# Kernel optimization log

Hardware: AMD Instinct MI355X
Metric: run time of the kernel (lower is better)

The kernel has to match this reference:

```python
import jax, jax.numpy as jnp
import numpy as np

DIM = 512
N_HEADS = 8
N_LAYERS = 2
N_BLOCKS = 9 * N_LAYERS
B = 8
L_LEN = V_LEN = A_LEN = 512
L_DIM, V_DIM, A_DIM = 768, 640, 205
N_CLASSES = 9


def setup_inputs() -> dict:
    key = jax.random.key(0)
    ks = jax.random.split(key, 16)
    s = 0.02
    return {
        'l': jax.random.normal(ks[0], (B, L_LEN, L_DIM), jnp.float32),
        'v': jax.random.normal(ks[1], (B, V_LEN, V_DIM), jnp.float32),
        'a': jax.random.normal(ks[2], (B, A_LEN, A_DIM), jnp.float32),
        'l_mask': jnp.ones((B, L_LEN), jnp.float32),
        'v_mask': jnp.ones((B, V_LEN), jnp.float32),
        'a_mask': jnp.ones((B, A_LEN), jnp.float32),
        'wl': jax.random.normal(ks[3], (L_DIM, DIM), jnp.float32) * s,
        'wv': jax.random.normal(ks[4], (V_DIM, DIM), jnp.float32) * s,
        'wa': jax.random.normal(ks[5], (A_DIM, DIM), jnp.float32) * s,
        'n1_g': jnp.ones((DIM,), jnp.float32),
        'n1_b': jnp.zeros((DIM,), jnp.float32),
        'proj_w': jax.random.normal(ks[6], (N_BLOCKS, DIM, DIM), jnp.float32) * s,
        'minus_w': jax.random.normal(ks[7], (N_BLOCKS, 2 * DIM, DIM), jnp.float32) * s,
        'n2_g': jnp.ones((N_BLOCKS, DIM), jnp.float32),
        'n2_b': jnp.zeros((N_BLOCKS, DIM), jnp.float32),
        'c': jnp.full((N_BLOCKS,), 0.1, jnp.float32),
        'clf_w': jax.random.normal(ks[8], (6 * N_LAYERS * DIM, N_CLASSES), jnp.float32) * s,
    }


def _ln(x, g, b, eps=1e-5):
    mu = jnp.mean(x, axis=-1, keepdims=True)
    var = jnp.mean((x - mu) ** 2, axis=-1, keepdims=True)
    return (x - mu) * jax.lax.rsqrt(var + eps) * g + b


def reference(l, v, a, l_mask, v_mask, a_mask, wl, wv, wa, n1_g, n1_b,
              proj_w, minus_w, n2_g, n2_b, c, clf_w):
    hd = DIM // N_HEADS
    inv_sqrt = 1.0 / np.sqrt(hd).astype(np.float32)

    def block(i, q_in, kv, mask, scores_prev):
        Bq, Lq, D = q_in.shape
        qh = q_in.reshape(Bq, Lq, N_HEADS, hd)
        kh = kv.reshape(Bq, kv.shape[1], N_HEADS, hd)  # k and v are the same raw tensor
        scores = jnp.einsum('bqhd,bkhd->bhqk', qh, kh) * inv_sqrt
        if scores_prev is not None:
            scores = scores + c[i] * scores_prev
        scores = scores - 1e8 * (1.0 - mask[:, None, None, :])
        att = jax.nn.softmax(scores, axis=-1)
        ctx = jnp.einsum('bhqk,bkhd->bqhd', att, kh).reshape(Bq, Lq, D)
        x = ctx @ proj_w[i]  # proj, no bias; dropout is identity (eval)
        out = _ln(jnp.concatenate([q_in, x], axis=-1) @ minus_w[i], n2_g[i], n2_b[i])
        return out, scores

    def stream(q0, kv, mask, off, outs):
        q, s = q0, None
        for j in range(N_LAYERS):
            q, s = block(off * N_LAYERS + j, q, kv, mask, s)
            outs.append(q)

    # Unify_Dimension
    lu = _ln(l @ wl, n1_g, n1_b)
    vu = _ln(v @ wv, n1_g, n1_b)
    au = _ln(a @ wa, n1_g, n1_b)

    l_list, v_list, a_list = [], [], []
    stream(lu, lu, l_mask, 0, l_list)
    stream(lu, vu, v_mask, 1, l_list)
    stream(lu, au, a_mask, 2, l_list)
    stream(vu, vu, v_mask, 3, v_list)
    stream(vu, lu, l_mask, 4, v_list)
    stream(vu, au, a_mask, 5, v_list)
    stream(au, au, a_mask, 6, a_list)
    stream(au, lu, l_mask, 7, a_list)
    stream(au, vu, v_mask, 8, a_list)

    lc = jnp.concatenate(l_list, axis=2)  # [B, l_len, 3*n_layers*dim]
    vc = jnp.concatenate(v_list, axis=2)
    ac = jnp.concatenate(a_list, axis=2)
    x = jnp.concatenate([lc, ac, vc], axis=1)  # note order: l, a, v (as in source)
    feats = jnp.concatenate([jnp.mean(x, axis=1), jnp.max(x, axis=1)], axis=1)
    return feats @ clf_w
```

## Files before the change

kernel.cpp:

```cpp
#include <hip/hip_runtime.h>
#include <cstdint>
#include <cstddef>

#define DEV __device__ __forceinline__

typedef __attribute__((ext_vector_type(8))) short short8;
typedef __attribute__((ext_vector_type(4))) float floatx4;
typedef unsigned short u16;
typedef unsigned int u32;

union Frag { short8 s8; uint4 u4; uint2 u2[2]; u16 us[8]; };

DEV float b2f(u16 u) { union { float f; u32 i; } v; v.i = ((u32)u) << 16; return v.f; }
DEV u16 f2b(float f) {
  union { float f; u32 i; } v; v.f = f; u32 x = v.i;
  return (u16)((x + 0x7fffu + ((x >> 16) & 1u)) >> 16);
}
DEV floatx4 mfma16(short8 a, short8 b, floatx4 c) {
  return __builtin_amdgcn_mfma_f32_16x16x32_bf16(a, b, c, 0, 0, 0);
}
DEV void gl_lds16(const u16* g, u16* l) {
  __builtin_amdgcn_global_load_lds(
      (const __attribute__((address_space(1))) void*)g,
      (__attribute__((address_space(3))) void*)l, 16, 0, 0);
}

__global__ void det_kernel(const u32* __restrict__ mask, int* __restrict__ flag)
{
  if (threadIdx.x == 0 && blockIdx.x == 0)
    *flag = (mask[0] == 0x3F803F80u) ? 0 : 1;
}

struct ConvArgs {
  const void* src[17];
  u16* dst[17];
  int n[17];
  int bstart[17];
};

__global__ __launch_bounds__(256, 4)
void convert_all_kernel(ConvArgs a, const int* __restrict__ flag)
{
  const int bid = blockIdx.x;
  int seg = 0;
  #pragma unroll
  for (int i = 1; i < 17; i++) if (bid >= a.bstart[i]) seg = i;
  const int n = a.n[seg];
  const int base = (bid - a.bstart[seg]) * 1024 + threadIdx.x * 4;
  if (base >= n) return;
  const int f32mode = *flag;
  if (base + 4 <= n) {
    union { uint2 v; u16 u[4]; } o;
    if (f32mode) {
      const float* s = (const float*)a.src[seg] + base;
      float4 f = *(const float4*)s;
      o.u[0] = f2b(f.x); o.u[1] = f2b(f.y); o.u[2] = f2b(f.z); o.u[3] = f2b(f.w);
    } else {
      o.v = *(const uint2*)((const u16*)a.src[seg] + base);
    }
    *(uint2*)(a.dst[seg] + base) = o.v;
  } else {
    for (int k = base; k < n; k++) {
      if (f32mode) a.dst[seg][k] = f2b(((const float*)a.src[seg])[k]);
      else         a.dst[seg][k] = ((const u16*)a.src[seg])[k];
    }
  }
}

__global__ __launch_bounds__(256, 2)
void transpose_kernel(const u16* __restrict__ S, u16* __restrict__ D,
                      int R, int dstStride, int srcZ, int dstZ)
{
  __shared__ u16 tile[64 * 72];
  const u16* src = S + (size_t)blockIdx.z * srcZ;
  u16* dst = D + (size_t)blockIdx.z * dstZ;
  const int r0 = blockIdx.x * 64, c0 = blockIdx.y * 64;
  const int t = threadIdx.x;
  const int row = t >> 2, cc = (t & 3) * 16;
  if (r0 + 64 <= R) {
    uint4 v0 = *(const uint4*)(src + (size_t)(r0 + row) * 512 + c0 + cc);
    uint4 v1 = *(const uint4*)(src + (size_t)(r0 + row) * 512 + c0 + cc + 8);
    *(uint4*)&tile[row * 72 + cc] = v0;
    *(uint4*)&tile[row * 72 + cc + 8] = v1;
  } else {
    bool ok = (r0 + row) < R;
    for (int j = 0; j < 16; j++)
      tile[row * 72 + cc + j] = ok ? src[(size_t)(r0 + row) * 512 + c0 + cc + j] : (u16)0;
  }
  __syncthreads();
  const int cl = t >> 2, rc = (t & 3) * 16;
  if (r0 + 64 <= dstStride) {
    union { uint4 v[2]; u16 u[16]; } o;
    #pragma unroll
    for (int j = 0; j < 16; j++) o.u[j] = tile[(rc + j) * 72 + cl];
    u16* gd = dst + (size_t)(c0 + cl) * dstStride + r0 + rc;
    *(uint4*)gd = o.v[0];
    *(uint4*)(gd + 8) = o.v[1];
  } else {
    for (int j = 0; j < 16; j++) {
      int rr = r0 + rc + j;
      if (rr < dstStride) dst[(size_t)(c0 + cl) * dstStride + rr] = tile[(rc + j) * 72 + cl];
    }
  }
}

__global__ __launch_bounds__(256, 4)
void gemm_kernel(const u16* __restrict__ A1, int lda1, int az1,
                 const u16* __restrict__ A2, int lda2, int az2,
                 const u16* __restrict__ B1, int ldb1, int bz1,
                 const u16* __restrict__ B2, int ldb2, int bz2,
                 u16* __restrict__ O, int oz,
                 int Ktot, int Ksplit, int KAvalid, int flags)
{
  __shared__ u16 gbuf[18432];
  u16* As = gbuf;
  u16* Bs = gbuf + 4096;

  const int z = blockIdx.z;
  const int m0 = blockIdx.x * 128, n0 = blockIdx.y * 128;
  const int t = threadIdx.x, w = t >> 6, l = t & 63, l15 = l & 15, quad = l >> 4;
  const int zA = (flags & 4) ? (z / 3) : z;
  const u16* A1p = A1 + (size_t)zA * az1;
  const u16* A2p = A2 ? (A2 + (size_t)z * az2) : nullptr;
  const u16* B1p = B1 + (size_t)z * bz1;
  const u16* B2p = B2 ? (B2 + (size_t)z * bz2) : nullptr;
  u16* Op = O + (size_t)z * oz;

  const int c0r = t >> 2;
  const int c0k = t & 3;
  u16* AsW = As + (size_t)t * 8;
  u16* BsW = Bs + (size_t)t * 8;

  floatx4 acc[4][4];
  #pragma unroll
  for (int i = 0; i < 4; i++)
    #pragma unroll
    for (int j = 0; j < 4; j++) {
      acc[i][j][0] = 0.f; acc[i][j][1] = 0.f; acc[i][j][2] = 0.f; acc[i][j][3] = 0.f;
    }

  const int nsteps = Ktot >> 5;
  const int mb = (w & 1) * 64, nb = (w >> 1) * 64;
  for (int ks = 0; ks < nsteps; ks++) {
    const int k0 = ks * 32;
    const bool s2 = (k0 >= Ksplit);
    const u16* Ab = s2 ? A2p : A1p;
    const int la = s2 ? lda2 : lda1;
    const u16* Bb = s2 ? B2p : B1p;
    const int lb = s2 ? ldb2 : ldb1;
    const int kl = k0 - (s2 ? Ksplit : 0);
    const u16* ga0 = Ab + (size_t)(m0 + c0r) * la + kl + c0k * 8;
    const u16* ga1 = Ab + (size_t)(m0 + c0r + 64) * la + kl + c0k * 8;
    const u16* gb0 = Bb + (size_t)(n0 + c0r) * lb + kl + c0k * 8;
    const u16* gb1 = Bb + (size_t)(n0 + c0r + 64) * lb + kl + c0k * 8;

    __syncthreads();
    gl_lds16(gb0, BsW);
    gl_lds16(gb1, BsW + 2048);
    if (!(flags & 1)) {
      gl_lds16(ga0, AsW);
      gl_lds16(ga1, AsW + 2048);
    } else {
      union { uint4 v; u16 u[8]; } tA[2];
      #pragma unroll
      for (int i = 0; i < 2; i++) {
        const u16* gp = i ? ga1 : ga0;
        for (int j = 0; j < 8; j++) {
          int k = kl + c0k * 8 + j;
          tA[i].u[j] = (k < KAvalid) ? gp[j] : (u16)0;
        }
      }
      *(uint4*)AsW = tA[0].v;
      *(uint4*)(AsW + 2048) = tA[1].v;
    }
    __syncthreads();

    Frag fa[4], fb[4];
    #pragma unroll
    for (int i = 0; i < 4; i++) {
      fa[i].u4 = *(const uint4*)&As[(mb + i * 16 + l15) * 32 + quad * 8];
      fb[i].u4 = *(const uint4*)&Bs[(nb + i * 16 + l15) * 32 + quad * 8];
    }
    #pragma unroll
    for (int i = 0; i < 4; i++)
      #pragma unroll
      for (int j = 0; j < 4; j++)
        acc[i][j] = mfma16(fa[i].s8, fb[j].s8, acc[i][j]);
  }

  __syncthreads();
  u16* strip = gbuf + w * 4608;
  if (!(flags & 2)) {
    #pragma unroll
    for (int i = 0; i < 4; i++)
      #pragma unroll
      for (int j = 0; j < 4; j++)
        #pragma unroll
        for (int rr = 0; rr < 4; rr++)
          strip[(i * 16 + quad * 4 + rr) * 72 + j * 16 + l15] = f2b(acc[i][j][rr]);
    const int row = l >> 3, cc = l & 7;
    #pragma unroll
    for (int i = 0; i < 8; i++) {
      uint4 v = *(const uint4*)&strip[(i * 8 + row) * 72 + cc * 8];
      *(uint4*)(Op + (size_t)(m0 + mb + i * 8 + row) * 512 + n0 + nb + cc * 8) = v;
    }
  } else {
    #pragma unroll
    for (int i = 0; i < 4; i++)
      #pragma unroll
      for (int j = 0; j < 4; j++)
        #pragma unroll
        for (int rr = 0; rr < 4; rr++)
          strip[(j * 16 + l15) * 72 + i * 16 + quad * 4 + rr] = f2b(acc[i][j][rr]);
    const int row = l >> 3, cc = l & 7;
    #pragma unroll
    for (int i = 0; i < 8; i++) {
      uint4 v = *(const uint4*)&strip[(i * 8 + row) * 72 + cc * 8];
      *(uint4*)(Op + (size_t)(n0 + nb + i * 8 + row) * 512 + m0 + mb + cc * 8) = v;
    }
  }
}

__global__ __launch_bounds__(256, 2)
void ln_kernel(const u16* __restrict__ In, u16* __restrict__ Out,
               const u16* __restrict__ G, const u16* __restrict__ Bb,
               int inz, int outz, int gz)
{
  const int z = blockIdx.y;
  const u16* in = In + (size_t)z * inz;
  u16* out = Out + (size_t)z * outz;
  const u16* g = G + (size_t)z * gz;
  const u16* bb = Bb + (size_t)z * gz;
  const int t = threadIdx.x, w = t >> 6, l = t & 63;
  const int row = blockIdx.x * 4 + w;
  union { uint4 v; u16 u[8]; } xv, gv, bv, ov;
  xv.v = *(const uint4*)(in + (size_t)row * 512 + l * 8);
  float x[8]; float s1 = 0.f, s2 = 0.f;
  #pragma unroll
  for (int j = 0; j < 8; j++) { x[j] = b2f(xv.u[j]); s1 += x[j]; s2 += x[j] * x[j]; }
  #pragma unroll
  for (int m = 1; m < 64; m <<= 1) { s1 += __shfl_xor(s1, m); s2 += __shfl_xor(s2, m); }
  float mu = s1 * (1.0f / 512.0f);
  float var = s2 * (1.0f / 512.0f) - mu * mu;
  float rs = rsqrtf(var + 1e-5f);
  gv.v = *(const uint4*)(g + l * 8);
  bv.v = *(const uint4*)(bb + l * 8);
  #pragma unroll
  for (int j = 0; j < 8; j++) ov.u[j] = f2b((x[j] - mu) * rs * b2f(gv.u[j]) + b2f(bv.u[j]));
  *(uint4*)(out + (size_t)row * 512 + l * 8) = ov.v;
}

__global__ __launch_bounds__(256, 2)
void flash_kernel(const u16* __restrict__ U, const u16* __restrict__ Ut,
                  const u16* __restrict__ OUT, u16* __restrict__ CTX,
                  const u16* __restrict__ mask_l, const u16* __restrict__ mask_v,
                  const u16* __restrict__ mask_a, const u16* __restrict__ cvec,
                  int layer)
{
  __shared__ u16 sm[26624];
  u16* madd = sm + 26112;
  const int QS = 0, PO = 8704, KS = 17408, KT = 21760;

  const int bx = blockIdx.x;
  const int qblk = bx / 576;
  const int rest = bx - qblk * 576;
  const int s = rest >> 6, b = (rest >> 3) & 7, h = rest & 7;
  const int t = threadIdx.x, w = t >> 6, l = t & 63, l15 = l & 15, quad = l >> 4;

  const int qm = s / 3;
  const int kvmodt[9] = {0, 1, 2, 1, 0, 2, 2, 0, 1};
  const int km = kvmodt[s];
  const size_t SZ = (size_t)4096 * 512;
  const float LOG2E = 1.44269504f;

  const u16* qptr; const u16* q0ptr = nullptr; float cv = 0.f;
  if (layer == 0) {
    qptr = U + (size_t)qm * SZ;
  } else {
    qptr = OUT + (size_t)(2 * s) * SZ;
    q0ptr = U + (size_t)qm * SZ;
    cv = b2f(cvec[2 * s + 1]);
  }
  const u16* kptr = U + (size_t)km * SZ;
  const u16* ktp = Ut + (size_t)(2 * km) * SZ + (size_t)b * 262144;
  const u16* mptr = (km == 0) ? mask_l : ((km == 1) ? mask_v : mask_a);
  const float msc = (1.0f + cv) * (-1e8f) * LOG2E;
  const float scl = 0.125f * LOG2E;

  for (int i = t; i < 512; i += 256)
    madd[i] = f2b((1.0f - b2f(mptr[b * 512 + i])) * msc);

  const size_t gqbase = (size_t)b * 512 * 512 + (size_t)(qblk * 128) * 512 + h * 64;
  const size_t gkbase = (size_t)b * 512 * 512 + h * 64;

  for (int i = 0; i < 4; i++) {
    int c = i * 256 + t, q = c >> 3, dc = c & 7;
    union { uint4 v; u16 u[8]; uint2 h2[2]; } raw, o;
    raw.v = *(const uint4*)(qptr + gqbase + (size_t)q * 512 + dc * 8);
    if (q0ptr) {
      union { uint4 v; u16 u[8]; } raw0;
      raw0.v = *(const uint4*)(q0ptr + gqbase + (size_t)q * 512 + dc * 8);
      #pragma unroll
      for (int j = 0; j < 8; j++) o.u[j] = f2b((b2f(raw.u[j]) + cv * b2f(raw0.u[j])) * scl);
    } else {
      #pragma unroll
      for (int j = 0; j < 8; j++) o.u[j] = f2b(b2f(raw.u[j]) * scl);
    }
    u16* dst = sm + QS + q * 68 + dc * 8;
    *(uint2*)dst = o.h2[0];
    *(uint2*)(dst + 4) = o.h2[1];
  }
  __syncthreads();

  Frag bfr[2][2];
  #pragma unroll
  for (int qt = 0; qt < 2; qt++)
    #pragma unroll
    for (int st = 0; st < 2; st++) {
      const u16* p = sm + QS + (w * 32 + qt * 16 + l15) * 68 + st * 32 + quad * 8;
      bfr[qt][st].u2[0] = *(const uint2*)p;
      bfr[qt][st].u2[1] = *(const uint2*)(p + 4);
    }

  float l_run[2] = {0.f, 0.f};
  floatx4 acc[4][2];
  #pragma unroll
  for (int i = 0; i < 2; i++)
    #pragma unroll
    for (int d = 0; d < 4; d++) { acc[d][i][0] = 0.f; acc[d][i][1] = 0.f; acc[d][i][2] = 0.f; acc[d][i][3] = 0.f; }

  for (int slab = 0; slab < 8; slab++) {
    for (int i = 0; i < 2; i++) {
      int c = i * 256 + t, kk = c >> 3, dc = c & 7;
      union { uint4 v; uint2 h2[2]; } raw;
      raw.v = *(const uint4*)(kptr + gkbase + (size_t)(slab * 64 + kk) * 512 + dc * 8);
      u16* ksd = sm + KS + kk * 68 + dc * 8;
      *(uint2*)ksd = raw.h2[0];
      *(uint2*)(ksd + 4) = raw.h2[1];
      union { uint4 v; uint2 h2[2]; } rawt;
      rawt.v = *(const uint4*)(ktp + (size_t)(h * 64 + kk) * 512 + slab * 64 + dc * 8);
      u16* ktd = sm + KT + kk * 68 + dc * 8;
      *(uint2*)ktd = rawt.h2[0];
      *(uint2*)(ktd + 4) = rawt.h2[1];
    }
    __syncthreads();

    Frag afr[4][2];
    #pragma unroll
    for (int kt = 0; kt < 4; kt++)
      #pragma unroll
      for (int st = 0; st < 2; st++) {
        const u16* p = sm + KS + (kt * 16 + l15) * 68 + st * 32 + quad * 8;
        afr[kt][st].u2[0] = *(const uint2*)p;
        afr[kt][st].u2[1] = *(const uint2*)(p + 4);
      }
    floatx4 cinit[4];
    #pragma unroll
    for (int kt = 0; kt < 4; kt++) {
      union { uint2 v; u16 u[4]; } mv;
      mv.v = *(const uint2*)&madd[slab * 64 + kt * 16 + quad * 4];
      #pragma unroll
      for (int rr = 0; rr < 4; rr++) cinit[kt][rr] = b2f(mv.u[rr]);
    }
    #pragma unroll
    for (int qt = 0; qt < 2; qt++) {
      floatx4 S[4];
      #pragma unroll
      for (int kt = 0; kt < 4; kt++) {
        floatx4 zz = cinit[kt];
        zz = mfma16(afr[kt][0].s8, bfr[qt][0].s8, zz);
        zz = mfma16(afr[kt][1].s8, bfr[qt][1].s8, zz);
        S[kt] = zz;
      }
      float ps = 0.f;
      #pragma unroll
      for (int kt = 0; kt < 4; kt++) {
        union { uint2 v; u16 u[4]; } pk;
        #pragma unroll
        for (int rr = 0; rr < 4; rr++) {
          float p = exp2f(S[kt][rr]);
          ps += p;
          pk.u[rr] = f2b(p);
        }
        *(uint2*)(sm + PO + (w * 32 + qt * 16 + l15) * 68 + kt * 16 + quad * 4) = pk.v;
      }
      ps += __shfl_xor(ps, 16);
      ps += __shfl_xor(ps, 32);
      l_run[qt] += ps;
    }

    Frag kfr[4][2], pfr[2][2];
    #pragma unroll
    for (int dt = 0; dt < 4; dt++)
      #pragma unroll
      for (int k2 = 0; k2 < 2; k2++) {
        const u16* p = sm + KT + (dt * 16 + l15) * 68 + k2 * 32 + quad * 8;
        kfr[dt][k2].u2[0] = *(const uint2*)p;
        kfr[dt][k2].u2[1] = *(const uint2*)(p + 4);
      }
    #pragma unroll
    for (int qt = 0; qt < 2; qt++)
      #pragma unroll
      for (int k2 = 0; k2 < 2; k2++) {
        const u16* p = sm + PO + (w * 32 + qt * 16 + l15) * 68 + k2 * 32 + quad * 8;
        pfr[qt][k2].u2[0] = *(const uint2*)p;
        pfr[qt][k2].u2[1] = *(const uint2*)(p + 4);
      }
    #pragma unroll
    for (int dt = 0; dt < 4; dt++)
      #pragma unroll
      for (int qt = 0; qt < 2; qt++) {
        acc[dt][qt] = mfma16(kfr[dt][0].s8, pfr[qt][0].s8, acc[dt][qt]);
        acc[dt][qt] = mfma16(kfr[dt][1].s8, pfr[qt][1].s8, acc[dt][qt]);
      }
    __syncthreads();
  }

  u16* strip = sm + KS + w * 2176;
  const size_t cbase = (size_t)s * SZ + (size_t)b * 512 * 512 + h * 64;
  #pragma unroll
  for (int qt = 0; qt < 2; qt++) {
    float rs = 1.0f / l_run[qt];
    #pragma unroll
    for (int dt = 0; dt < 4; dt++) {
      union { uint2 v; u16 u[4]; } pk;
      #pragma unroll
      for (int rr = 0; rr < 4; rr++) pk.u[rr] = f2b(acc[dt][qt][rr] * rs);
      *(uint2*)(strip + l15 * 68 + dt * 16 + quad * 4) = pk.v;
    }
    const int row = l >> 2, cc = l & 3;
    const u16* sp = strip + row * 68 + cc * 16;
    uint4 v0 = *(const uint4*)sp;
    uint4 v1 = *(const uint4*)(sp + 8);
    int q = qblk * 128 + w * 32 + qt * 16 + row;
    u16* gd = CTX + cbase + (size_t)q * 512 + cc * 16;
    *(uint4*)gd = v0;
    *(uint4*)(gd + 8) = v1;
  }
}

__global__ __launch_bounds__(256, 2)
void feats_kernel(const u16* __restrict__ OUT, float* __restrict__ F)
{
  const int b = blockIdx.y, t = threadIdx.x;
  const int jl = t & 63, qp = t >> 6;
  const int j = blockIdx.x * 64 + jl;
  const int e = j >> 9, col = j & 511, sub = e >> 1, lay = e & 1;
  const int g0[3] = {0, 6, 3};
  float sum = 0.f, mx = -3e38f;
  for (int gi = 0; gi < 3; gi++) {
    int sid = g0[gi] + sub;
    const u16* base = OUT + ((size_t)(sid * 2 + lay) * 4096 + b * 512 + qp * 128) * 512 + col;
    #pragma unroll 8
    for (int q = 0; q < 128; q++) {
      float v = b2f(base[(size_t)q * 512]);
      sum += v;
      mx = fmaxf(mx, v);
    }
  }
  __shared__ float rsm[256], rmm[256];
  rsm[t] = sum; rmm[t] = mx;
  __syncthreads();
  if (qp == 0) {
    float ts = rsm[jl] + rsm[64 + jl] + rsm[128 + jl] + rsm[192 + jl];
    float tm = fmaxf(fmaxf(rmm[jl], rmm[64 + jl]), fmaxf(rmm[128 + jl], rmm[192 + jl]));
    F[(size_t)b * 6144 + j] = ts * (1.0f / 1536.0f);
    F[(size_t)b * 6144 + 3072 + j] = tm;
  }
}

__global__ __launch_bounds__(256, 2)
void clf_kernel(const float* __restrict__ F, const u16* __restrict__ Wc,
                void* __restrict__ OutD, const int* __restrict__ flag)
{
  const int b = blockIdx.x, t = threadIdx.x;
  float pa[9];
  #pragma unroll
  for (int c = 0; c < 9; c++) pa[c] = 0.f;
  for (int j = t; j < 6144; j += 256) {
    float f = F[(size_t)b * 6144 + j];
    #pragma unroll
    for (int c = 0; c < 9; c++) pa[c] += f * b2f(Wc[(size_t)j * 9 + c]);
  }
  __shared__ float red[9 * 256];
  #pragma unroll
  for (int c = 0; c < 9; c++) red[c * 256 + t] = pa[c];
  __syncthreads();
  for (int sft = 128; sft > 0; sft >>= 1) {
    if (t < sft) {
      #pragma unroll
      for (int c = 0; c < 9; c++) red[c * 256 + t] += red[c * 256 + t + sft];
    }
    __syncthreads();
  }
  if (t < 9) {
    if (*flag) ((float*)OutD)[b * 9 + t] = red[t * 256];
    else       ((u16*)OutD)[b * 9 + t] = f2b(red[t * 256]);
  }
}

extern "C" void kernel_launch(void* const* d_in, const int* in_sizes, int n_in,
                              void* d_out, int out_size, void* d_ws, size_t ws_size,
                              hipStream_t stream)
{
  (void)n_in; (void)out_size; (void)ws_size;
  const size_t SZ = (size_t)4096 * 512;

  u16* Wp  = (u16*)d_ws;
  u16* U   = Wp;
  u16* Y   = U + 3 * SZ;
  u16* CTX = Y + 9 * SZ;
  u16* OUTb = CTX + 9 * SZ;
  u16* BtM = OUTb + 18 * SZ;
  u16* W2t = BtM + (size_t)18 * 512 * 1024;
  u16* wlT = W2t + (size_t)18 * 512 * 512;
  u16* wvT = wlT + (size_t)512 * 768;
  u16* waT = wvT + (size_t)512 * 640;
  u16* sm0 = waT + (size_t)512 * 224;
  float* F = (float*)sm0;  sm0 += (size_t)2 * 8 * 6144;
  int* flag = (int*)sm0;   sm0 += 2;
  u16* cml  = sm0; sm0 += 4096;
  u16* cmv  = sm0; sm0 += 4096;
  u16* cma  = sm0; sm0 += 4096;
  u16* cn1g = sm0; sm0 += 512;
  u16* cn1b = sm0; sm0 += 512;
  u16* cn2g = sm0; sm0 += 9216;
  u16* cn2b = sm0; sm0 += 9216;
  u16* ccv  = sm0; sm0 += 32;
  u16* ccw  = sm0; sm0 += 55296;
  u16* cl  = CTX;
  u16* cv2 = CTX + 3145728;
  u16* ca  = CTX + 5767168;
  u16* cmw = OUTb;
  u16* cpw = OUTb + 9437184;
  u16* cwl = OUTb + 14155776;
  u16* cwv = cwl + 393216;
  u16* cwa = cwv + 327680;
  u16* Ut = OUTb + SZ;

  det_kernel<<<1, 64, 0, stream>>>((const u32*)d_in[3], flag);

  ConvArgs ca_args;
  u16* cdst[17] = {cl, cv2, ca, cml, cmv, cma, cwl, cwv, cwa, cn1g, cn1b,
                   cpw, cmw, cn2g, cn2b, ccv, ccw};
  int btot = 0;
  for (int i = 0; i < 17; i++) {
    ca_args.src[i] = d_in[i];
    ca_args.dst[i] = cdst[i];
    ca_args.n[i] = in_sizes[i];
    ca_args.bstart[i] = btot;
    btot += (in_sizes[i] + 1023) / 1024;
  }
  convert_all_kernel<<<btot, 256, 0, stream>>>(ca_args, flag);

  transpose_kernel<<<dim3(12, 8, 1), 256, 0, stream>>>(cwl, wlT, 768, 768, 0, 0);
  transpose_kernel<<<dim3(10, 8, 1), 256, 0, stream>>>(cwv, wvT, 640, 640, 0, 0);
  transpose_kernel<<<dim3(4, 8, 1), 256, 0, stream>>>(cwa, waT, 205, 224, 0, 0);
  transpose_kernel<<<dim3(16, 8, 18), 256, 0, stream>>>(cmw, BtM, 1024, 1024, 1024 * 512, 512 * 1024);

  gemm_kernel<<<dim3(4, 4, 18), 256, 0, stream>>>(
      cpw, 512, 512 * 512, nullptr, 0, 0,
      BtM + 512, 1024, 512 * 1024, nullptr, 0, 0,
      W2t, 512 * 512, 512, 512, 512, 2);

  gemm_kernel<<<dim3(32, 4, 1), 256, 0, stream>>>(
      cl, 768, 0, nullptr, 0, 0, wlT, 768, 0, nullptr, 0, 0,
      Y, 0, 768, 768, 768, 0);
  gemm_kernel<<<dim3(32, 4, 1), 256, 0, stream>>>(
      cv2, 640, 0, nullptr, 0, 0, wvT, 640, 0, nullptr, 0, 0,
      Y + SZ, 0, 640, 640, 640, 0);
  gemm_kernel<<<dim3(32, 4, 1), 256, 0, stream>>>(
      ca, 205, 0, nullptr, 0, 0, waT, 224, 0, nullptr, 0, 0,
      Y + 2 * SZ, 0, 224, 224, 205, 1);
  ln_kernel<<<dim3(1024, 3), 256, 0, stream>>>(Y, U, cn1g, cn1b, (int)SZ, (int)SZ, 0);

  for (int m = 0; m < 3; m++)
    transpose_kernel<<<dim3(8, 8, 8), 256, 0, stream>>>(
        U + (size_t)m * SZ, Ut + (size_t)(2 * m) * SZ, 512, 512, 262144, 262144);

  for (int layer = 0; layer < 2; layer++) {
    flash_kernel<<<2304, 256, 0, stream>>>(U, Ut, OUTb, CTX, cml, cmv, cma, ccv, layer);
    const u16* A1 = layer ? OUTb : U;
    int az1 = layer ? (int)(2 * SZ) : (int)SZ;
    int fl = layer ? 0 : 4;
    gemm_kernel<<<dim3(32, 4, 9), 256, 0, stream>>>(
        A1, 512, az1, CTX, 512, (int)SZ,
        BtM + (size_t)layer * 512 * 1024, 1024, 2 * 512 * 1024,
        W2t + (size_t)layer * 512 * 512, 512, 2 * 512 * 512,
        Y, (int)SZ, 1024, 512, 1024, fl);
    ln_kernel<<<dim3(1024, 9), 256, 0, stream>>>(
        Y, OUTb + (size_t)layer * SZ, cn2g + layer * 512, cn2b + layer * 512,
        (int)SZ, (int)(2 * SZ), 1024);
  }

  feats_kernel<<<dim3(48, 8), 256, 0, stream>>>(OUTb, F);
  clf_kernel<<<8, 256, 0, stream>>>(F, ccw, d_out, flag);
}
```

Before: 631.8 us.

## Load K fragments directly from global, alias P into Q buffer, shrink LDS

The flash attention kernel now reads the K operand fragments for the QK^T MFMA straight from global memory into registers instead of staging them through shared memory. It also writes the probability tile over the Q staging area, which is dead once the Q fragments are in registers. Together these cut LDS use roughly in half, and launch bounds rise to 4 blocks per CU. Block index decoding now places the four query blocks of one (stream, batch, head) next to each other, so they share K/V in cache, and the exp values are truncated to bf16 with a bit mask before summing and packing. The risks are uncoalesced global loads for K fragments, register pressure under the tighter launch bound, and a small precision change from truncating instead of rounding.

```diff
diff --git a/kernel.cpp b/kernel.cpp
--- a/kernel.cpp
+++ b/kernel.cpp
@@ -250,21 +250,21 @@
   *(uint4*)(out + (size_t)row * 512 + l * 8) = ov.v;
 }
 
-__global__ __launch_bounds__(256, 2)
+__global__ __launch_bounds__(256, 4)
 void flash_kernel(const u16* __restrict__ U, const u16* __restrict__ Ut,
                   const u16* __restrict__ OUT, u16* __restrict__ CTX,
                   const u16* __restrict__ mask_l, const u16* __restrict__ mask_v,
                   const u16* __restrict__ mask_a, const u16* __restrict__ cvec,
                   int layer)
 {
-  __shared__ u16 sm[26624];
-  u16* madd = sm + 26112;
-  const int QS = 0, PO = 8704, KS = 17408, KT = 21760;
+  __shared__ u16 sm[13568];
+  const int QP = 0, KT = 8704;
+  u16* madd = sm + 13056;
 
   const int bx = blockIdx.x;
-  const int qblk = bx / 576;
-  const int rest = bx - qblk * 576;
-  const int s = rest >> 6, b = (rest >> 3) & 7, h = rest & 7;
+  const int qblk = bx & 3;
+  const int rest = bx >> 2;
+  const int h = rest & 7, b = (rest >> 3) & 7, s = rest >> 6;
   const int t = threadIdx.x, w = t >> 6, l = t & 63, l15 = l & 15, quad = l >> 4;
 
   const int qm = s / 3;
@@ -306,7 +306,7 @@
       #pragma unroll
       for (int j = 0; j < 8; j++) o.u[j] = f2b(b2f(raw.u[j]) * scl);
     }
-    u16* dst = sm + QS + q * 68 + dc * 8;
+    u16* dst = sm + QP + q * 68 + dc * 8;
     *(uint2*)dst = o.h2[0];
     *(uint2*)(dst + 4) = o.h2[1];
   }
@@ -317,7 +317,7 @@
   for (int qt = 0; qt < 2; qt++)
     #pragma unroll
     for (int st = 0; st < 2; st++) {
-      const u16* p = sm + QS + (w * 32 + qt * 16 + l15) * 68 + st * 32 + quad * 8;
+      const u16* p = sm + QP + (w * 32 + qt * 16 + l15) * 68 + st * 32 + quad * 8;
       bfr[qt][st].u2[0] = *(const uint2*)p;
       bfr[qt][st].u2[1] = *(const uint2*)(p + 4);
     }
@@ -329,31 +329,25 @@
     #pragma unroll
     for (int d = 0; d < 4; d++) { acc[d][i][0] = 0.f; acc[d][i][1] = 0.f; acc[d][i][2] = 0.f; acc[d][i][3] = 0.f; }
 
+  const u16* kfb = kptr + gkbase + (size_t)l15 * 512 + quad * 8;
+
   for (int slab = 0; slab < 8; slab++) {
+    #pragma unroll
     for (int i = 0; i < 2; i++) {
-      int c = i * 256 + t, kk = c >> 3, dc = c & 7;
-      union { uint4 v; uint2 h2[2]; } raw;
-      raw.v = *(const uint4*)(kptr + gkbase + (size_t)(slab * 64 + kk) * 512 + dc * 8);
-      u16* ksd = sm + KS + kk * 68 + dc * 8;
-      *(uint2*)ksd = raw.h2[0];
-      *(uint2*)(ksd + 4) = raw.h2[1];
+      int c = i * 256 + t, d = c >> 3, kc = c & 7;
       union { uint4 v; uint2 h2[2]; } rawt;
-      rawt.v = *(const uint4*)(ktp + (size_t)(h * 64 + kk) * 512 + slab * 64 + dc * 8);
-      u16* ktd = sm + KT + kk * 68 + dc * 8;
+      rawt.v = *(const uint4*)(ktp + (size_t)(h * 64 + d) * 512 + slab * 64 + kc * 8);
+      u16* ktd = sm + KT + d * 68 + kc * 8;
       *(uint2*)ktd = rawt.h2[0];
       *(uint2*)(ktd + 4) = rawt.h2[1];
     }
-    __syncthreads();
-
     Frag afr[4][2];
+    const u16* kslab = kfb + (size_t)slab * 64 * 512;
     #pragma unroll
     for (int kt = 0; kt < 4; kt++)
       #pragma unroll
-      for (int st = 0; st < 2; st++) {
-        const u16* p = sm + KS + (kt * 16 + l15) * 68 + st * 32 + quad * 8;
-        afr[kt][st].u2[0] = *(const uint2*)p;
-        afr[kt][st].u2[1] = *(const uint2*)(p + 4);
-      }
+      for (int st = 0; st < 2; st++)
+        afr[kt][st].u4 = *(const uint4*)(kslab + (size_t)(kt * 16) * 512 + st * 32);
     floatx4 cinit[4];
     #pragma unroll
     for (int kt = 0; kt < 4; kt++) {
@@ -362,6 +356,8 @@
       #pragma unroll
       for (int rr = 0; rr < 4; rr++) cinit[kt][rr] = b2f(mv.u[rr]);
     }
+    __syncthreads();
+
     #pragma unroll
     for (int qt = 0; qt < 2; qt++) {
       floatx4 S[4];
@@ -375,14 +371,19 @@
       float ps = 0.f;
       #pragma unroll
       for (int kt = 0; kt < 4; kt++) {
-        union { uint2 v; u16 u[4]; } pk;
+        u32 pi[4];
         #pragma unroll
         for (int rr = 0; rr < 4; rr++) {
-          float p = exp2f(S[kt][rr]);
-          ps += p;
-          pk.u[rr] = f2b(p);
+          union { float f; u32 i; } pv;
+          pv.f = exp2f(S[kt][rr]);
+          pi[rr] = pv.i & 0xffff0000u;
+          pv.i = pi[rr];
+          ps += pv.f;
         }
-        *(uint2*)(sm + PO + (w * 32 + qt * 16 + l15) * 68 + kt * 16 + quad * 4) = pk.v;
+        uint2 pk;
+        pk.x = (pi[0] >> 16) | pi[1];
+        pk.y = (pi[2] >> 16) | pi[3];
+        *(uint2*)(sm + QP + (w * 32 + qt * 16 + l15) * 68 + kt * 16 + quad * 4) = pk;
       }
       ps += __shfl_xor(ps, 16);
       ps += __shfl_xor(ps, 32);
@@ -402,7 +403,7 @@
     for (int qt = 0; qt < 2; qt++)
       #pragma unroll
       for (int k2 = 0; k2 < 2; k2++) {
-        const u16* p = sm + PO + (w * 32 + qt * 16 + l15) * 68 + k2 * 32 + quad * 8;
+        const u16* p = sm + QP + (w * 32 + qt * 16 + l15) * 68 + k2 * 32 + quad * 8;
         pfr[qt][k2].u2[0] = *(const uint2*)p;
         pfr[qt][k2].u2[1] = *(const uint2*)(p + 4);
       }
@@ -416,7 +417,7 @@
     __syncthreads();
   }
 
-  u16* strip = sm + KS + w * 2176;
+  u16* strip = sm + KT + w * 1088;
   const size_t cbase = (size_t)s * SZ + (size_t)b * 512 * 512 + h * 64;
   #pragma unroll
   for (int qt = 0; qt < 2; qt++) {
```

Measured after the change: 634.6 us. No clear change (+0.4%).
